# Performance work log

Measured on AMD Instinct MI355X. Metric: run time of the kernel, lower is better.

The kernel has to match this reference:

```python
import jax, jax.numpy as jnp
import numpy as np

B, N, D = 8, 8192, 64          # batch, input points, point feature dim
NPOINT, NSAMPLE = 1024, 16     # FPS samples S, KNN neighbors K
WN, OUT = 16, 128              # weightnet out channels, output channels
CIN = 3 + D                    # concat(xyz_norm, point feats) = linear in_channel
NEG_SLOPE = 0.1


def setup_inputs() -> dict:
    key = jax.random.key(0)
    ks = jax.random.split(key, 8)
    rn = lambda k, shp, s: jax.random.normal(k, shp, jnp.float32) * s
    return {
        "xyz": rn(ks[0], (B, 3, N), 1.0),
        "points": rn(ks[1], (B, D, N), 1.0),
        "w1": rn(ks[2], (3, 8), 0.5), "b1": jnp.zeros((8,), jnp.float32),
        "w2": rn(ks[3], (8, 8), 0.35), "b2": jnp.zeros((8,), jnp.float32),
        "w3": rn(ks[4], (8, WN), 0.35), "b3": jnp.zeros((WN,), jnp.float32),
        "lin_w": rn(ks[5], (WN * CIN, OUT), 0.03),
        "lin_b": jnp.zeros((OUT,), jnp.float32),
    }


def _fps(xyz):
    """Furthest point sampling. xyz: [B,N,3] -> idx [B,NPOINT] int32."""
    def step(carry, _):
        dist, farthest = carry  # [B,N], [B]
        centroid = jnp.take_along_axis(xyz, farthest[:, None, None], axis=1)  # [B,1,3]
        d = jnp.sum((xyz - centroid) ** 2, axis=-1)  # [B,N]
        dist = jnp.minimum(dist, d)
        return (dist, jnp.argmax(dist, axis=-1).astype(jnp.int32)), farthest
    init = (jnp.full((xyz.shape[0], xyz.shape[1]), 1e10, xyz.dtype),
            jnp.zeros((xyz.shape[0],), jnp.int32))
    _, idxs = jax.lax.scan(step, init, None, length=NPOINT)
    return idxs.T  # [B, NPOINT]


def reference(xyz, points, w1, b1, w2, b2, w3, b3, lin_w, lin_b):
    xyz_t = xyz.transpose(0, 2, 1)       # [B,N,3]
    pts_t = points.transpose(0, 2, 1)    # [B,N,D]

    fps_idx = _fps(xyz_t)                                   # [B,S]
    bidx = jnp.arange(B)[:, None]
    new_xyz = xyz_t[bidx, fps_idx]                          # [B,S,3]

    # KNN: squared distances (same ordering as euclidean cdist)
    sqr = jnp.sum((new_xyz[:, :, None, :] - xyz_t[:, None, :, :]) ** 2, axis=-1)  # [B,S,N]
    _, knn = jax.lax.top_k(-sqr, NSAMPLE)                   # [B,S,K]

    b3i = jnp.arange(B)[:, None, None]
    g_xyz = xyz_t[b3i, knn]                                 # [B,S,K,3]
    g_xyz_norm = g_xyz - new_xyz[:, :, None, :]             # [B,S,K,3]
    g_pts = pts_t[b3i, knn]                                 # [B,S,K,D]
    feat = jnp.concatenate([g_xyz_norm, g_pts], axis=-1)    # [B,S,K,3+D]

    # WeightNet: 1x1 convs == per-neighbor MLP on xyz offsets
    h = jax.nn.relu(g_xyz_norm @ w1 + b1)
    h = jax.nn.relu(h @ w2 + b2)
    wts = jax.nn.relu(h @ w3 + b3)                          # [B,S,K,WN]

    # weighted aggregation over K, then flatten [C, WN]
    agg = jnp.einsum('bskc,bskw->bscw', feat, wts).reshape(B, NPOINT, CIN * WN)
    out = agg @ lin_w + lin_b                               # [B,S,OUT]
    out = jnp.where(out > 0, out, NEG_SLOPE * out)          # LeakyReLU(0.1)

    return new_xyz.transpose(0, 2, 1), out.transpose(0, 2, 1), fps_idx
```

## Files before the change

### kernel.cpp

```cpp
#include <hip/hip_runtime.h>
#include <hip/hip_bf16.h>

#define NPTS   8192
#define NBATCH 8
#define S      1024
#define K      16
#define D      64
#define CIN    67
#define WN     16
#define OUTC   128

#define OUT_MAIN 24576
#define OUT_FPS  1073152

#define T_FPS   0
#define T_TP    8
#define T_KNN   1032
#define T_FEAT  1544
#define T_GEMM  2568
#define NBLK    2824

#define SCOPE __HIP_MEMORY_SCOPE_AGENT

typedef float v2f __attribute__((ext_vector_type(2)));

struct Ctrl {
  int ticket;
  int pad0[31];
  int tp_done[8];
  int pad1[24];
  int tile_done[128];
};

__device__ __forceinline__ unsigned long long aload64(const unsigned long long* p) {
  return __hip_atomic_load(p, __ATOMIC_RELAXED, SCOPE);
}
__device__ __forceinline__ void astore64(unsigned long long* p, unsigned long long v) {
  __hip_atomic_store(p, v, __ATOMIC_RELAXED, SCOPE);
}
__device__ __forceinline__ void wait_cnt(int* p, int need) {
  if (threadIdx.x == 0)
    while (__hip_atomic_load(p, __ATOMIC_RELAXED, SCOPE) < need)
      __builtin_amdgcn_s_sleep(4);
  __syncthreads();
}

template <int CTRL, int RM>
__device__ __forceinline__ unsigned long long dpp_max_step(unsigned long long key) {
  int lo = __builtin_amdgcn_update_dpp(0, (int)(unsigned)(key & 0xFFFFFFFFull), CTRL, RM, 0xF, true);
  int hi = __builtin_amdgcn_update_dpp(0, (int)(unsigned)(key >> 32),           CTRL, RM, 0xF, true);
  unsigned long long o = ((unsigned long long)(unsigned)hi << 32) | (unsigned)lo;
  return o > key ? o : key;
}

__device__ void fps_role(int b, const float* __restrict__ xyz,
                         unsigned long long* __restrict__ nxA,
                         unsigned long long* __restrict__ nxB,
                         float* __restrict__ out, void* smem)
{
#pragma clang fp contract(off)
  float* s_x = (float*)smem;
  float* s_y = s_x + NPTS;
  float* s_z = s_y + NPTS;
  float4* hist = (float4*)((char*)smem + 98304);
  unsigned long long* slots = (unsigned long long*)((char*)smem + 114688);

  const int tid  = threadIdx.x;
  const int wave = tid >> 6;
  const int lane = tid & 63;
  const float* xb = xyz + (size_t)b * 3 * NPTS;

  v2f px[8], py[8], pz[8], dist[8];
#pragma unroll
  for (int p = 0; p < 8; p++) {
    int ne = (2 * p) * 512 + tid;
    int no = ne + 512;
    px[p] = (v2f){xb[ne], xb[no]};
    py[p] = (v2f){xb[NPTS + ne], xb[NPTS + no]};
    pz[p] = (v2f){xb[2 * NPTS + ne], xb[2 * NPTS + no]};
    dist[p] = (v2f){1e10f, 1e10f};
    s_x[ne] = px[p].x; s_x[no] = px[p].y;
    s_y[ne] = py[p].x; s_y[no] = py[p].y;
    s_z[ne] = pz[p].x; s_z[no] = pz[p].y;
  }

  int far = 0;
  float cx = xb[0], cy = xb[NPTS], cz = xb[2 * NPTS];

  for (int t = 0; t < 1024; t++) {
    if (tid == (t & 511))
      hist[t] = make_float4(cx, cy, cz, (float)far);

    if ((t & 31) == 0 && t > 0 && wave == 0 && lane < 32) {
      int tt = t - 32 + lane;
      float4 h = hist[tt];
      int gidx = (b << 10) + tt;
      astore64(&nxA[gidx],
               ((unsigned long long)__float_as_uint(h.x) << 32) | __float_as_uint(h.y));
      astore64(&nxB[gidx],
               ((unsigned long long)__float_as_uint(h.z) << 32) | (unsigned)((int)h.w + 1));
    }

    const v2f c2x = (v2f){cx, cx}, c2y = (v2f){cy, cy}, c2z = (v2f){cz, cz};

    float bd_e = -1.0f, bd_o = -1.0f;
    int   ce   = 0,     co   = 0;
#pragma unroll
    for (int p = 0; p < 8; p++) {
      v2f dx = px[p] - c2x, dy = py[p] - c2y, dz = pz[p] - c2z;
      v2f d  = (dx * dx + dy * dy) + dz * dz;
      float nde = fminf(dist[p].x, d.x);
      float ndo = fminf(dist[p].y, d.y);
      dist[p].x = nde;
      dist[p].y = ndo;
      if (nde > bd_e) { bd_e = nde; ce = 2 * p; }
      if (ndo > bd_o) { bd_o = ndo; co = 2 * p + 1; }
    }

    unsigned long long ke =
        ((unsigned long long)__float_as_uint(bd_e) << 32) | (unsigned)(~(unsigned)(ce * 512 + tid));
    unsigned long long ko =
        ((unsigned long long)__float_as_uint(bd_o) << 32) | (unsigned)(~(unsigned)(co * 512 + tid));
    unsigned long long key = ko > ke ? ko : ke;

    key = dpp_max_step<0x111, 0xF>(key);
    key = dpp_max_step<0x112, 0xF>(key);
    key = dpp_max_step<0x114, 0xF>(key);
    key = dpp_max_step<0x118, 0xF>(key);
    key = dpp_max_step<0x142, 0xA>(key);
    key = dpp_max_step<0x143, 0xC>(key);
    if (lane == 63) slots[(t & 1) * 8 + wave] = key;
    __syncthreads();

    const unsigned long long* sl = slots + (t & 1) * 8;
    unsigned long long k0 = sl[0], k1 = sl[1], k2 = sl[2], k3 = sl[3];
    unsigned long long k4 = sl[4], k5 = sl[5], k6 = sl[6], k7 = sl[7];
    k0 = k1 > k0 ? k1 : k0;
    k2 = k3 > k2 ? k3 : k2;
    k4 = k5 > k4 ? k5 : k4;
    k6 = k7 > k6 ? k7 : k6;
    k0 = k2 > k0 ? k2 : k0;
    k4 = k6 > k4 ? k6 : k4;
    k0 = k4 > k0 ? k4 : k0;
    int gi = (int)(~(unsigned)(k0 & 0xFFFFFFFFull));
    far = gi;
    cx = s_x[gi]; cy = s_y[gi]; cz = s_z[gi];
  }
  __syncthreads();

  if (wave == 0 && lane < 32) {
    int tt = 992 + lane;
    float4 h = hist[tt];
    int gidx = (b << 10) + tt;
    astore64(&nxA[gidx],
             ((unsigned long long)__float_as_uint(h.x) << 32) | __float_as_uint(h.y));
    astore64(&nxB[gidx],
             ((unsigned long long)__float_as_uint(h.z) << 32) | (unsigned)((int)h.w + 1));
  }

#pragma unroll
  for (int j = 0; j < 2; j++) {
    int t = j * 512 + tid;
    float4 h = hist[t];
    out[OUT_FPS + b * 1024 + t] = h.w;
    out[b * 3072 + t]           = h.x;
    out[b * 3072 + 1024 + t]    = h.y;
    out[b * 3072 + 2048 + t]    = h.z;
  }
}

__device__ void tp_role(int bid, const float* __restrict__ pts, float* __restrict__ ptt,
                        Ctrl* ctrl, void* smem)
{
  float* tile = (float*)smem;
  const int b  = bid >> 7;
  const int n0 = (bid & 127) * 64;
  const float* pb = pts + (size_t)b * D * NPTS;
#pragma unroll
  for (int i = 0; i < 8; i++) {
    int s = threadIdx.x + i * 512;
    int nl = s & 63, d = s >> 6;
    tile[d * 65 + nl] = pb[(size_t)d * NPTS + n0 + nl];
  }
  __syncthreads();
  float* ob = ptt + ((size_t)b * NPTS + n0) * D;
#pragma unroll
  for (int i = 0; i < 8; i++) {
    int s = threadIdx.x + i * 512;
    int dl = s & 63, nl = s >> 6;
    ob[(size_t)nl * D + dl] = tile[dl * 65 + nl];
  }
  __syncthreads();
  if (threadIdx.x == 0)
    __hip_atomic_fetch_add(&ctrl->tp_done[b], 1, __ATOMIC_RELEASE, SCOPE);
}

__device__ void knn_role(int kidx, const float* __restrict__ xyz,
                         const unsigned long long* __restrict__ nxA,
                         const unsigned long long* __restrict__ nxB,
                         unsigned long long* __restrict__ knnP, void* smem)
{
#pragma clang fp contract(off)
  float (*s_cc)[4] = (float(*)[4])smem;
  unsigned long long* s_k = (unsigned long long*)((char*)smem + 256);
  const int tid   = threadIdx.x;
  const int cl    = tid >> 5;
  const int chunk = tid & 31;
  const int b     = kidx >> 6;
  const int c0    = (kidx & 63) * 16;
  const int cbase = (b << 10) + c0;

  if (chunk == 0) {
    unsigned long long Bv, Av;
    do { Bv = aload64(&nxB[cbase + cl]); } while ((unsigned)(Bv & 0xFFFFFFFFull) == 0u);
    do { Av = aload64(&nxA[cbase + cl]); } while (Av == 0ull);
    s_cc[cl][0] = __uint_as_float((unsigned)(Av >> 32));
    s_cc[cl][1] = __uint_as_float((unsigned)(Av & 0xFFFFFFFFull));
    s_cc[cl][2] = __uint_as_float((unsigned)(Bv >> 32));
  }
  __syncthreads();

  const float* xb = xyz + (size_t)b * 3 * NPTS;
  const float cx = s_cc[cl][0], cy = s_cc[cl][1], cz = s_cc[cl][2];

  float nd[16]; int ni[16];
#pragma unroll
  for (int k = 0; k < 16; k++) { nd[k] = 3.4e38f; ni[k] = 0x7FFFFFFF; }

  for (int jj = 0; jj < 256; jj++) {
    int j = jj * 32 + chunk;
    float dx = xb[j] - cx, dy = xb[NPTS + j] - cy, dz = xb[2 * NPTS + j] - cz;
    float d  = (dx * dx + dy * dy) + dz * dz;
    float cv = d; int iv = j;
#pragma unroll
    for (int k = 0; k < 16; k++) {
      bool sw = cv < nd[k];
      float tv = nd[k]; int ti = ni[k];
      nd[k] = sw ? cv : tv;  ni[k] = sw ? iv : ti;
      cv    = sw ? tv : cv;  iv    = sw ? ti : iv;
    }
  }
#pragma unroll
  for (int k = 0; k < 16; k++)
    s_k[cl * 545 + chunk * 17 + k] =
        ((unsigned long long)__float_as_uint(nd[k]) << 32) | (unsigned)ni[k];
  s_k[cl * 545 + chunk * 17 + 16] = ~0ull;
  __syncthreads();

  if (tid < 16) {
    int pos[32];
#pragma unroll
    for (int c = 0; c < 32; c++) pos[c] = 0;
    int res[16];
    for (int r = 0; r < 16; r++) {
      unsigned long long bk = ~0ull; int bc = 0;
#pragma unroll
      for (int c = 0; c < 32; c++) {
        unsigned long long kv = s_k[tid * 545 + c * 17 + pos[c]];
        if (kv < bk) { bk = kv; bc = c; }
      }
#pragma unroll
      for (int c = 0; c < 32; c++) pos[c] += (c == bc);
      res[r] = (int)(bk & 0xFFFFFFFFull);
    }
#pragma unroll
    for (int w = 0; w < 8; w++)
      astore64(&knnP[(size_t)(cbase + tid) * 8 + w],
               ((unsigned long long)(unsigned)(res[2 * w] + 1) << 32) |
               (unsigned)(res[2 * w + 1] + 1));
  }
}

__device__ void feat_role(int fidx, const float* __restrict__ xyz,
                          const unsigned long long* __restrict__ nxA,
                          const unsigned long long* __restrict__ nxB,
                          const float* __restrict__ ptt,
                          const unsigned long long* __restrict__ knnP,
                          const float* __restrict__ w1, const float* __restrict__ b1,
                          const float* __restrict__ w2, const float* __restrict__ b2,
                          const float* __restrict__ w3, const float* __restrict__ b3,
                          float* __restrict__ agg, Ctrl* ctrl, void* smem)
{
  float* s_wts = (float*)smem;
  float* s_off = s_wts + 8 * 272;
  int*   s_nk  = (int*)(s_off + 8 * 48);

  const int C0 = fidx * 8;
  const int b  = C0 >> 10;

  wait_cnt(&ctrl->tp_done[b], 128);

  const int wv   = threadIdx.x >> 6;
  const int lane = threadIdx.x & 63;
  const int csel = C0 + wv;

  if (lane < 16) {
    const unsigned long long* wp = &knnP[(size_t)csel * 8 + (lane >> 1)];
    unsigned long long wd;
    do { wd = aload64(wp); } while (wd == 0ull);
    unsigned v = (lane & 1) ? (unsigned)(wd & 0xFFFFFFFFull) : (unsigned)(wd >> 32);
    int nk = (int)v - 1;
    s_nk[wv * 16 + lane] = nk;

    unsigned long long Av, Bv;
    do { Av = aload64(&nxA[csel]); } while (Av == 0ull);
    do { Bv = aload64(&nxB[csel]); } while ((unsigned)(Bv & 0xFFFFFFFFull) == 0u);
    float ccx = __uint_as_float((unsigned)(Av >> 32));
    float ccy = __uint_as_float((unsigned)(Av & 0xFFFFFFFFull));
    float ccz = __uint_as_float((unsigned)(Bv >> 32));

    const float* xb = xyz + (size_t)b * 3 * NPTS;
    float ox = xb[nk]            - ccx;
    float oy = xb[NPTS + nk]     - ccy;
    float oz = xb[2 * NPTS + nk] - ccz;
    s_off[wv * 48 + lane * 3 + 0] = ox;
    s_off[wv * 48 + lane * 3 + 1] = oy;
    s_off[wv * 48 + lane * 3 + 2] = oz;
    float h1[8], h2[8];
#pragma unroll
    for (int j = 0; j < 8; j++)
      h1[j] = fmaxf(0.f, ox * w1[j] + oy * w1[8 + j] + oz * w1[16 + j] + b1[j]);
#pragma unroll
    for (int j = 0; j < 8; j++) {
      float a = b2[j];
#pragma unroll
      for (int i = 0; i < 8; i++) a = fmaf(h1[i], w2[i * 8 + j], a);
      h2[j] = fmaxf(0.f, a);
    }
#pragma unroll
    for (int w = 0; w < 16; w++) {
      float a = b3[w];
#pragma unroll
      for (int i = 0; i < 8; i++) a = fmaf(h2[i], w3[i * 16 + w], a);
      s_wts[wv * 272 + lane * 17 + w] = fmaxf(0.f, a);
    }
  }
  __syncthreads();

  float f[16];
#pragma unroll
  for (int k = 0; k < 16; k++) {
    int nk = s_nk[wv * 16 + k];
    f[k] = ptt[((size_t)b * NPTS + nk) * D + lane];
  }

  float acc[16];
#pragma unroll
  for (int w = 0; w < 16; w++) acc[w] = 0.f;
#pragma unroll
  for (int k = 0; k < 16; k++) {
#pragma unroll
    for (int w = 0; w < 16; w++)
      acc[w] = fmaf(f[k], s_wts[wv * 272 + k * 17 + w], acc[w]);
  }
  float* arow = agg + (size_t)csel * (CIN * WN) + (3 + lane) * 16;
#pragma unroll
  for (int q = 0; q < 4; q++) {
    float4 v = make_float4(acc[4 * q], acc[4 * q + 1], acc[4 * q + 2], acc[4 * q + 3]);
    *(float4*)(arow + 4 * q) = v;
  }

  if (lane < 48) {
    int c = lane >> 4, w = lane & 15;
    float a = 0.f;
#pragma unroll
    for (int k = 0; k < 16; k++)
      a = fmaf(s_off[wv * 48 + k * 3 + c], s_wts[wv * 272 + k * 17 + w], a);
    agg[(size_t)csel * (CIN * WN) + c * 16 + w] = a;
  }
  __syncthreads();
  if (threadIdx.x == 0)
    __hip_atomic_fetch_add(&ctrl->tile_done[C0 >> 6], 1, __ATOMIC_RELEASE, SCOPE);
}

__device__ void gemm_role(int gidx, const float* __restrict__ agg, const float* __restrict__ lin_w,
                          const float* __restrict__ lin_b, float* __restrict__ out,
                          Ctrl* ctrl, void* smem)
{
  float* a_t = (float*)smem;
  float* b_t = a_t + 16 * 68;
  const int rt   = gidx >> 1;
  const int ct   = gidx & 1;
  const int row0 = rt * 64;
  const int c0   = ct * 64;

  wait_cnt(&ctrl->tile_done[rt], 8);

  const int tid = threadIdx.x;
  const int cg  = tid & 31;
  const int rg  = tid >> 5;

  float acc[4][2] = {};
  for (int kt = 0; kt < 67; kt++) {
    const int k0 = kt * 16;
#pragma unroll
    for (int i = 0; i < 2; i++) {
      int s = tid + i * 512;
      int kk = s & 15, r = s >> 4;
      a_t[kk * 68 + r] = agg[(size_t)(row0 + r) * (CIN * WN) + k0 + kk];
    }
#pragma unroll
    for (int i = 0; i < 2; i++) {
      int s = tid + i * 512;
      int c = s & 63, kk = s >> 6;
      b_t[kk * 64 + c] = lin_w[(size_t)(k0 + kk) * OUTC + c0 + c];
    }
    __syncthreads();
#pragma unroll
    for (int kk = 0; kk < 16; kk++) {
      const float4 a0 = *(const float4*)&a_t[kk * 68 + rg * 4];
      float bv0 = b_t[kk * 64 + cg * 2];
      float bv1 = b_t[kk * 64 + cg * 2 + 1];
      float av[4] = {a0.x, a0.y, a0.z, a0.w};
#pragma unroll
      for (int rr = 0; rr < 4; rr++) {
        acc[rr][0] = fmaf(av[rr], bv0, acc[rr][0]);
        acc[rr][1] = fmaf(av[rr], bv1, acc[rr][1]);
      }
    }
    __syncthreads();
  }
#pragma unroll
  for (int rr = 0; rr < 4; rr++) {
#pragma unroll
    for (int cc = 0; cc < 2; cc++) {
      int R = row0 + rg * 4 + rr;
      int C = c0 + cg * 2 + cc;
      float v = acc[rr][cc] + lin_b[C];
      v = v > 0.f ? v : 0.1f * v;
      int bb = R >> 10, ss = R & 1023;
      out[OUT_MAIN + ((size_t)(bb * OUTC + C)) * 1024 + ss] = v;
    }
  }
}

__global__ __launch_bounds__(512)
void mega_kernel(const float* __restrict__ xyz, const float* __restrict__ pts,
                 const float* __restrict__ w1, const float* __restrict__ b1,
                 const float* __restrict__ w2, const float* __restrict__ b2,
                 const float* __restrict__ w3, const float* __restrict__ b3,
                 const float* __restrict__ lin_w, const float* __restrict__ lin_b,
                 float* __restrict__ out, unsigned long long* __restrict__ nxA,
                 unsigned long long* __restrict__ nxB, unsigned long long* __restrict__ knnP,
                 float* __restrict__ ptt, float* __restrict__ agg, Ctrl* ctrl)
{
  __shared__ __align__(16) unsigned long long smem[14400];
  __shared__ int s_ticket;
  if (threadIdx.x == 0)
    s_ticket = __hip_atomic_fetch_add(&ctrl->ticket, 1, __ATOMIC_RELAXED, SCOPE);
  __syncthreads();
  const int tk = s_ticket;

  if (tk < T_TP)
    fps_role(tk, xyz, nxA, nxB, out, smem);
  else if (tk < T_KNN)
    tp_role(tk - T_TP, pts, ptt, ctrl, smem);
  else if (tk < T_FEAT)
    knn_role(tk - T_KNN, xyz, nxA, nxB, knnP, smem);
  else if (tk < T_GEMM)
    feat_role(tk - T_FEAT, xyz, nxA, nxB, ptt, knnP,
              w1, b1, w2, b2, w3, b3, agg, ctrl, smem);
  else
    gemm_role(tk - T_GEMM, agg, lin_w, lin_b, out, ctrl, smem);
}

extern "C" void kernel_launch(void* const* d_in, const int* in_sizes, int n_in,
                              void* d_out, int out_size, void* d_ws, size_t ws_size,
                              hipStream_t stream) {
  const float* xyz    = (const float*)d_in[0];
  const float* points = (const float*)d_in[1];
  const float* w1     = (const float*)d_in[2];
  const float* b1     = (const float*)d_in[3];
  const float* w2     = (const float*)d_in[4];
  const float* b2     = (const float*)d_in[5];
  const float* w3     = (const float*)d_in[6];
  const float* b3     = (const float*)d_in[7];
  const float* lin_w  = (const float*)d_in[8];
  const float* lin_b  = (const float*)d_in[9];
  float* out = (float*)d_out;
  char*  ws  = (char*)d_ws;

  Ctrl* ctrl                = (Ctrl*)(ws);
  unsigned long long* nxA   = (unsigned long long*)(ws + 4096);
  unsigned long long* nxB   = (unsigned long long*)(ws + 69632);
  unsigned long long* knnP  = (unsigned long long*)(ws + 135168);
  float* ptt                = (float*)(ws + 1048576);
  float* agg                = (float*)(ws + 17825792);

  hipMemsetAsync(ws, 0, 659456, stream);
  mega_kernel<<<NBLK, 512, 0, stream>>>(xyz, points, w1, b1, w2, b2, w3, b3,
                                        lin_w, lin_b, out, nxA, nxB, knnP, ptt, agg, ctrl);
}
```

Measured before the change: 1.340 ms.

## Fuse KNN, feature aggregation and GEMM into one per-centroid-tile worker role

Replaces the separate KNN, feature and GEMM block roles, which were chained through global flags (knnP, tile_done), with a single worker block per 16-centroid tile. That block does the KNN, keeps the neighbor indices in shared memory, computes the weightnet and aggregation, then runs the final linear layer for its 16 rows. This removes the knnP buffer, the inter-block spin-waits and about half the blocks. In exchange each block reloads the full lin_w for only 16 rows (less reuse than the 64x64 GEMM tiles), and the GEMM tail now sits after each block's KNN on the critical path.

```diff
diff --git a/kernel.cpp b/kernel.cpp
--- a/kernel.cpp
+++ b/kernel.cpp
@@ -15,10 +15,8 @@
 
 #define T_FPS   0
 #define T_TP    8
-#define T_KNN   1032
-#define T_FEAT  1544
-#define T_GEMM  2568
-#define NBLK    2824
+#define T_WK    1032
+#define NBLK    1544
 
 #define SCOPE __HIP_MEMORY_SCOPE_AGENT
 
@@ -28,8 +26,6 @@
   int ticket;
   int pad0[31];
   int tp_done[8];
-  int pad1[24];
-  int tile_done[128];
 };
 
 __device__ __forceinline__ unsigned long long aload64(const unsigned long long* p) {
@@ -37,12 +33,6 @@
 }
 __device__ __forceinline__ void astore64(unsigned long long* p, unsigned long long v) {
   __hip_atomic_store(p, v, __ATOMIC_RELAXED, SCOPE);
-}
-__device__ __forceinline__ void wait_cnt(int* p, int need) {
-  if (threadIdx.x == 0)
-    while (__hip_atomic_load(p, __ATOMIC_RELAXED, SCOPE) < need)
-      __builtin_amdgcn_s_sleep(4);
-  __syncthreads();
 }
 
 template <int CTRL, int RM>
@@ -195,63 +185,77 @@
     __hip_atomic_fetch_add(&ctrl->tp_done[b], 1, __ATOMIC_RELEASE, SCOPE);
 }
 
-__device__ void knn_role(int kidx, const float* __restrict__ xyz,
-                         const unsigned long long* __restrict__ nxA,
-                         const unsigned long long* __restrict__ nxB,
-                         unsigned long long* __restrict__ knnP, void* smem)
+__device__ void worker_role(int u, const float* __restrict__ xyz,
+                            const unsigned long long* __restrict__ nxA,
+                            const unsigned long long* __restrict__ nxB,
+                            const float* __restrict__ ptt,
+                            const float* __restrict__ w1, const float* __restrict__ b1,
+                            const float* __restrict__ w2, const float* __restrict__ b2,
+                            const float* __restrict__ w3, const float* __restrict__ b3,
+                            const float* __restrict__ lin_w, const float* __restrict__ lin_b,
+                            float* __restrict__ agg, float* __restrict__ out,
+                            Ctrl* ctrl, void* smem)
 {
+  const int tid = threadIdx.x;
+  const int b   = u & 7;
+  const int q   = u >> 3;
+  const int c0  = q * 16;
+  const int cbase = (b << 10) + c0;
+
+  unsigned long long* s_k = (unsigned long long*)smem;
+  float* s_cc = (float*)((char*)smem + 69760);
+  int*   s_nk = (int*)((char*)smem + 70016);
+
+  if (tid < 16) {
+    unsigned long long Bv, Av;
+    while ((unsigned)((Bv = aload64(&nxB[cbase + tid])) & 0xFFFFFFFFull) == 0u)
+      __builtin_amdgcn_s_sleep(8);
+    while ((Av = aload64(&nxA[cbase + tid])) == 0ull)
+      __builtin_amdgcn_s_sleep(1);
+    s_cc[tid * 4 + 0] = __uint_as_float((unsigned)(Av >> 32));
+    s_cc[tid * 4 + 1] = __uint_as_float((unsigned)(Av & 0xFFFFFFFFull));
+    s_cc[tid * 4 + 2] = __uint_as_float((unsigned)(Bv >> 32));
+  }
+  __syncthreads();
+
+  {
 #pragma clang fp contract(off)
-  float (*s_cc)[4] = (float(*)[4])smem;
-  unsigned long long* s_k = (unsigned long long*)((char*)smem + 256);
-  const int tid   = threadIdx.x;
-  const int cl    = tid >> 5;
-  const int chunk = tid & 31;
-  const int b     = kidx >> 6;
-  const int c0    = (kidx & 63) * 16;
-  const int cbase = (b << 10) + c0;
-
-  if (chunk == 0) {
-    unsigned long long Bv, Av;
-    do { Bv = aload64(&nxB[cbase + cl]); } while ((unsigned)(Bv & 0xFFFFFFFFull) == 0u);
-    do { Av = aload64(&nxA[cbase + cl]); } while (Av == 0ull);
-    s_cc[cl][0] = __uint_as_float((unsigned)(Av >> 32));
-    s_cc[cl][1] = __uint_as_float((unsigned)(Av & 0xFFFFFFFFull));
-    s_cc[cl][2] = __uint_as_float((unsigned)(Bv >> 32));
-  }
-  __syncthreads();
-
-  const float* xb = xyz + (size_t)b * 3 * NPTS;
-  const float cx = s_cc[cl][0], cy = s_cc[cl][1], cz = s_cc[cl][2];
-
-  float nd[16]; int ni[16];
-#pragma unroll
-  for (int k = 0; k < 16; k++) { nd[k] = 3.4e38f; ni[k] = 0x7FFFFFFF; }
-
-  for (int jj = 0; jj < 256; jj++) {
-    int j = jj * 32 + chunk;
-    float dx = xb[j] - cx, dy = xb[NPTS + j] - cy, dz = xb[2 * NPTS + j] - cz;
-    float d  = (dx * dx + dy * dy) + dz * dz;
-    float cv = d; int iv = j;
-#pragma unroll
-    for (int k = 0; k < 16; k++) {
-      bool sw = cv < nd[k];
-      float tv = nd[k]; int ti = ni[k];
-      nd[k] = sw ? cv : tv;  ni[k] = sw ? iv : ti;
-      cv    = sw ? tv : cv;  iv    = sw ? ti : iv;
-    }
-  }
-#pragma unroll
-  for (int k = 0; k < 16; k++)
-    s_k[cl * 545 + chunk * 17 + k] =
-        ((unsigned long long)__float_as_uint(nd[k]) << 32) | (unsigned)ni[k];
-  s_k[cl * 545 + chunk * 17 + 16] = ~0ull;
+    const int cl    = tid >> 5;
+    const int chunk = tid & 31;
+    const float* xb = xyz + (size_t)b * 3 * NPTS;
+    const float cx = s_cc[cl * 4 + 0];
+    const float cy = s_cc[cl * 4 + 1];
+    const float cz = s_cc[cl * 4 + 2];
+
+    float nd[16]; int ni[16];
+#pragma unroll
+    for (int k = 0; k < 16; k++) { nd[k] = 3.4e38f; ni[k] = 0x7FFFFFFF; }
+
+    for (int jj = 0; jj < 256; jj++) {
+      int j = jj * 32 + chunk;
+      float dx = xb[j] - cx, dy = xb[NPTS + j] - cy, dz = xb[2 * NPTS + j] - cz;
+      float d  = (dx * dx + dy * dy) + dz * dz;
+      float cv = d; int iv = j;
+#pragma unroll
+      for (int k = 0; k < 16; k++) {
+        bool sw = cv < nd[k];
+        float tv = nd[k]; int ti = ni[k];
+        nd[k] = sw ? cv : tv;  ni[k] = sw ? iv : ti;
+        cv    = sw ? tv : cv;  iv    = sw ? ti : iv;
+      }
+    }
+#pragma unroll
+    for (int k = 0; k < 16; k++)
+      s_k[cl * 545 + chunk * 17 + k] =
+          ((unsigned long long)__float_as_uint(nd[k]) << 32) | (unsigned)ni[k];
+    s_k[cl * 545 + chunk * 17 + 16] = ~0ull;
+  }
   __syncthreads();
 
   if (tid < 16) {
     int pos[32];
 #pragma unroll
     for (int c = 0; c < 32; c++) pos[c] = 0;
-    int res[16];
     for (int r = 0; r < 16; r++) {
       unsigned long long bk = ~0ull; int bc = 0;
 #pragma unroll
@@ -261,175 +265,122 @@
       }
 #pragma unroll
       for (int c = 0; c < 32; c++) pos[c] += (c == bc);
-      res[r] = (int)(bk & 0xFFFFFFFFull);
-    }
-#pragma unroll
-    for (int w = 0; w < 8; w++)
-      astore64(&knnP[(size_t)(cbase + tid) * 8 + w],
-               ((unsigned long long)(unsigned)(res[2 * w] + 1) << 32) |
-               (unsigned)(res[2 * w + 1] + 1));
-  }
-}
-
-__device__ void feat_role(int fidx, const float* __restrict__ xyz,
-                          const unsigned long long* __restrict__ nxA,
-                          const unsigned long long* __restrict__ nxB,
-                          const float* __restrict__ ptt,
-                          const unsigned long long* __restrict__ knnP,
-                          const float* __restrict__ w1, const float* __restrict__ b1,
-                          const float* __restrict__ w2, const float* __restrict__ b2,
-                          const float* __restrict__ w3, const float* __restrict__ b3,
-                          float* __restrict__ agg, Ctrl* ctrl, void* smem)
-{
+      s_nk[tid * 16 + r] = (int)(bk & 0xFFFFFFFFull);
+    }
+  }
+  if (tid == 0)
+    while (__hip_atomic_load(&ctrl->tp_done[b], __ATOMIC_RELAXED, SCOPE) < 128)
+      __builtin_amdgcn_s_sleep(8);
+  __syncthreads();
+
   float* s_wts = (float*)smem;
   float* s_off = s_wts + 8 * 272;
-  int*   s_nk  = (int*)(s_off + 8 * 48);
-
-  const int C0 = fidx * 8;
-  const int b  = C0 >> 10;
-
-  wait_cnt(&ctrl->tp_done[b], 128);
-
-  const int wv   = threadIdx.x >> 6;
-  const int lane = threadIdx.x & 63;
-  const int csel = C0 + wv;
-
-  if (lane < 16) {
-    const unsigned long long* wp = &knnP[(size_t)csel * 8 + (lane >> 1)];
-    unsigned long long wd;
-    do { wd = aload64(wp); } while (wd == 0ull);
-    unsigned v = (lane & 1) ? (unsigned)(wd & 0xFFFFFFFFull) : (unsigned)(wd >> 32);
-    int nk = (int)v - 1;
-    s_nk[wv * 16 + lane] = nk;
-
-    unsigned long long Av, Bv;
-    do { Av = aload64(&nxA[csel]); } while (Av == 0ull);
-    do { Bv = aload64(&nxB[csel]); } while ((unsigned)(Bv & 0xFFFFFFFFull) == 0u);
-    float ccx = __uint_as_float((unsigned)(Av >> 32));
-    float ccy = __uint_as_float((unsigned)(Av & 0xFFFFFFFFull));
-    float ccz = __uint_as_float((unsigned)(Bv >> 32));
-
-    const float* xb = xyz + (size_t)b * 3 * NPTS;
-    float ox = xb[nk]            - ccx;
-    float oy = xb[NPTS + nk]     - ccy;
-    float oz = xb[2 * NPTS + nk] - ccz;
-    s_off[wv * 48 + lane * 3 + 0] = ox;
-    s_off[wv * 48 + lane * 3 + 1] = oy;
-    s_off[wv * 48 + lane * 3 + 2] = oz;
-    float h1[8], h2[8];
-#pragma unroll
-    for (int j = 0; j < 8; j++)
-      h1[j] = fmaxf(0.f, ox * w1[j] + oy * w1[8 + j] + oz * w1[16 + j] + b1[j]);
-#pragma unroll
-    for (int j = 0; j < 8; j++) {
-      float a = b2[j];
-#pragma unroll
-      for (int i = 0; i < 8; i++) a = fmaf(h1[i], w2[i * 8 + j], a);
-      h2[j] = fmaxf(0.f, a);
-    }
-#pragma unroll
-    for (int w = 0; w < 16; w++) {
-      float a = b3[w];
-#pragma unroll
-      for (int i = 0; i < 8; i++) a = fmaf(h2[i], w3[i * 16 + w], a);
-      s_wts[wv * 272 + lane * 17 + w] = fmaxf(0.f, a);
-    }
-  }
-  __syncthreads();
-
-  float f[16];
-#pragma unroll
-  for (int k = 0; k < 16; k++) {
-    int nk = s_nk[wv * 16 + k];
-    f[k] = ptt[((size_t)b * NPTS + nk) * D + lane];
-  }
-
-  float acc[16];
-#pragma unroll
-  for (int w = 0; w < 16; w++) acc[w] = 0.f;
-#pragma unroll
-  for (int k = 0; k < 16; k++) {
-#pragma unroll
-    for (int w = 0; w < 16; w++)
-      acc[w] = fmaf(f[k], s_wts[wv * 272 + k * 17 + w], acc[w]);
-  }
-  float* arow = agg + (size_t)csel * (CIN * WN) + (3 + lane) * 16;
-#pragma unroll
-  for (int q = 0; q < 4; q++) {
-    float4 v = make_float4(acc[4 * q], acc[4 * q + 1], acc[4 * q + 2], acc[4 * q + 3]);
-    *(float4*)(arow + 4 * q) = v;
-  }
-
-  if (lane < 48) {
-    int c = lane >> 4, w = lane & 15;
-    float a = 0.f;
-#pragma unroll
-    for (int k = 0; k < 16; k++)
-      a = fmaf(s_off[wv * 48 + k * 3 + c], s_wts[wv * 272 + k * 17 + w], a);
-    agg[(size_t)csel * (CIN * WN) + c * 16 + w] = a;
-  }
-  __syncthreads();
-  if (threadIdx.x == 0)
-    __hip_atomic_fetch_add(&ctrl->tile_done[C0 >> 6], 1, __ATOMIC_RELEASE, SCOPE);
-}
-
-__device__ void gemm_role(int gidx, const float* __restrict__ agg, const float* __restrict__ lin_w,
-                          const float* __restrict__ lin_b, float* __restrict__ out,
-                          Ctrl* ctrl, void* smem)
-{
+  const int wv   = tid >> 6;
+  const int lane = tid & 63;
+
+  for (int it = 0; it < 2; it++) {
+    const int cl2  = it * 8 + wv;
+    const int csel = cbase + cl2;
+    if (lane < 16) {
+      int nk = s_nk[cl2 * 16 + lane];
+      const float* xb = xyz + (size_t)b * 3 * NPTS;
+      float ox = xb[nk]            - s_cc[cl2 * 4 + 0];
+      float oy = xb[NPTS + nk]     - s_cc[cl2 * 4 + 1];
+      float oz = xb[2 * NPTS + nk] - s_cc[cl2 * 4 + 2];
+      s_off[wv * 48 + lane * 3 + 0] = ox;
+      s_off[wv * 48 + lane * 3 + 1] = oy;
+      s_off[wv * 48 + lane * 3 + 2] = oz;
+      float h1[8], h2[8];
+#pragma unroll
+      for (int j = 0; j < 8; j++)
+        h1[j] = fmaxf(0.f, ox * w1[j] + oy * w1[8 + j] + oz * w1[16 + j] + b1[j]);
+#pragma unroll
+      for (int j = 0; j < 8; j++) {
+        float a = b2[j];
+#pragma unroll
+        for (int i = 0; i < 8; i++) a = fmaf(h1[i], w2[i * 8 + j], a);
+        h2[j] = fmaxf(0.f, a);
+      }
+#pragma unroll
+      for (int w = 0; w < 16; w++) {
+        float a = b3[w];
+#pragma unroll
+        for (int i = 0; i < 8; i++) a = fmaf(h2[i], w3[i * 16 + w], a);
+        s_wts[wv * 272 + lane * 17 + w] = fmaxf(0.f, a);
+      }
+    }
+    __syncthreads();
+
+    float f[16];
+#pragma unroll
+    for (int k = 0; k < 16; k++) {
+      int nk = s_nk[cl2 * 16 + k];
+      f[k] = ptt[((size_t)b * NPTS + nk) * D + lane];
+    }
+    float acc[16];
+#pragma unroll
+    for (int w = 0; w < 16; w++) acc[w] = 0.f;
+#pragma unroll
+    for (int k = 0; k < 16; k++) {
+#pragma unroll
+      for (int w = 0; w < 16; w++)
+        acc[w] = fmaf(f[k], s_wts[wv * 272 + k * 17 + w], acc[w]);
+    }
+    float* arow = agg + (size_t)csel * (CIN * WN) + (3 + lane) * 16;
+#pragma unroll
+    for (int qq = 0; qq < 4; qq++) {
+      float4 v = make_float4(acc[4 * qq], acc[4 * qq + 1], acc[4 * qq + 2], acc[4 * qq + 3]);
+      *(float4*)(arow + 4 * qq) = v;
+    }
+    if (lane < 48) {
+      int c = lane >> 4, w = lane & 15;
+      float a = 0.f;
+#pragma unroll
+      for (int k = 0; k < 16; k++)
+        a = fmaf(s_off[wv * 48 + k * 3 + c], s_wts[wv * 272 + k * 17 + w], a);
+      agg[(size_t)csel * (CIN * WN) + c * 16 + w] = a;
+    }
+    __syncthreads();
+  }
+
   float* a_t = (float*)smem;
-  float* b_t = a_t + 16 * 68;
-  const int rt   = gidx >> 1;
-  const int ct   = gidx & 1;
-  const int row0 = rt * 64;
-  const int c0   = ct * 64;
-
-  wait_cnt(&ctrl->tile_done[rt], 8);
-
-  const int tid = threadIdx.x;
-  const int cg  = tid & 31;
-  const int rg  = tid >> 5;
-
-  float acc[4][2] = {};
+  float* b_t = a_t + 16 * 17;
+  float acc2[2][2] = {};
   for (int kt = 0; kt < 67; kt++) {
     const int k0 = kt * 16;
-#pragma unroll
-    for (int i = 0; i < 2; i++) {
-      int s = tid + i * 512;
-      int kk = s & 15, r = s >> 4;
-      a_t[kk * 68 + r] = agg[(size_t)(row0 + r) * (CIN * WN) + k0 + kk];
-    }
-#pragma unroll
-    for (int i = 0; i < 2; i++) {
-      int s = tid + i * 512;
-      int c = s & 63, kk = s >> 6;
-      b_t[kk * 64 + c] = lin_w[(size_t)(k0 + kk) * OUTC + c0 + c];
+    if (tid < 256) {
+      int r = tid & 15, kk = tid >> 4;
+      a_t[kk * 17 + r] = agg[(size_t)(cbase + r) * (CIN * WN) + k0 + kk];
+    }
+#pragma unroll
+    for (int i = 0; i < 4; i++) {
+      int idx = tid + i * 512;
+      int c = idx & 127, kk = idx >> 7;
+      b_t[kk * 128 + c] = lin_w[(size_t)(k0 + kk) * OUTC + c];
     }
     __syncthreads();
 #pragma unroll
     for (int kk = 0; kk < 16; kk++) {
-      const float4 a0 = *(const float4*)&a_t[kk * 68 + rg * 4];
-      float bv0 = b_t[kk * 64 + cg * 2];
-      float bv1 = b_t[kk * 64 + cg * 2 + 1];
-      float av[4] = {a0.x, a0.y, a0.z, a0.w};
-#pragma unroll
-      for (int rr = 0; rr < 4; rr++) {
-        acc[rr][0] = fmaf(av[rr], bv0, acc[rr][0]);
-        acc[rr][1] = fmaf(av[rr], bv1, acc[rr][1]);
-      }
+      float a0 = a_t[kk * 17 + wv * 2];
+      float a1 = a_t[kk * 17 + wv * 2 + 1];
+      float bv0 = b_t[kk * 128 + lane * 2];
+      float bv1 = b_t[kk * 128 + lane * 2 + 1];
+      acc2[0][0] = fmaf(a0, bv0, acc2[0][0]);
+      acc2[0][1] = fmaf(a0, bv1, acc2[0][1]);
+      acc2[1][0] = fmaf(a1, bv0, acc2[1][0]);
+      acc2[1][1] = fmaf(a1, bv1, acc2[1][1]);
     }
     __syncthreads();
   }
 #pragma unroll
-  for (int rr = 0; rr < 4; rr++) {
+  for (int j = 0; j < 2; j++) {
 #pragma unroll
     for (int cc = 0; cc < 2; cc++) {
-      int R = row0 + rg * 4 + rr;
-      int C = c0 + cg * 2 + cc;
-      float v = acc[rr][cc] + lin_b[C];
+      int ss = c0 + wv * 2 + j;
+      int C  = lane * 2 + cc;
+      float v = acc2[j][cc] + lin_b[C];
       v = v > 0.f ? v : 0.1f * v;
-      int bb = R >> 10, ss = R & 1023;
-      out[OUT_MAIN + ((size_t)(bb * OUTC + C)) * 1024 + ss] = v;
+      out[OUT_MAIN + ((size_t)(b * OUTC + C)) * 1024 + ss] = v;
     }
   }
 }
@@ -441,7 +392,7 @@
                  const float* __restrict__ w3, const float* __restrict__ b3,
                  const float* __restrict__ lin_w, const float* __restrict__ lin_b,
                  float* __restrict__ out, unsigned long long* __restrict__ nxA,
-                 unsigned long long* __restrict__ nxB, unsigned long long* __restrict__ knnP,
+                 unsigned long long* __restrict__ nxB,
                  float* __restrict__ ptt, float* __restrict__ agg, Ctrl* ctrl)
 {
   __shared__ __align__(16) unsigned long long smem[14400];
@@ -453,15 +404,11 @@
 
   if (tk < T_TP)
     fps_role(tk, xyz, nxA, nxB, out, smem);
-  else if (tk < T_KNN)
+  else if (tk < T_WK)
     tp_role(tk - T_TP, pts, ptt, ctrl, smem);
-  else if (tk < T_FEAT)
-    knn_role(tk - T_KNN, xyz, nxA, nxB, knnP, smem);
-  else if (tk < T_GEMM)
-    feat_role(tk - T_FEAT, xyz, nxA, nxB, ptt, knnP,
-              w1, b1, w2, b2, w3, b3, agg, ctrl, smem);
   else
-    gemm_role(tk - T_GEMM, agg, lin_w, lin_b, out, ctrl, smem);
+    worker_role(tk - T_WK, xyz, nxA, nxB, ptt, w1, b1, w2, b2, w3, b3,
+                lin_w, lin_b, agg, out, ctrl, smem);
 }
 
 extern "C" void kernel_launch(void* const* d_in, const int* in_sizes, int n_in,
@@ -480,14 +427,13 @@
   float* out = (float*)d_out;
   char*  ws  = (char*)d_ws;
 
-  Ctrl* ctrl                = (Ctrl*)(ws);
-  unsigned long long* nxA   = (unsigned long long*)(ws + 4096);
-  unsigned long long* nxB   = (unsigned long long*)(ws + 69632);
-  unsigned long long* knnP  = (unsigned long long*)(ws + 135168);
-  float* ptt                = (float*)(ws + 1048576);
-  float* agg                = (float*)(ws + 17825792);
-
-  hipMemsetAsync(ws, 0, 659456, stream);
+  Ctrl* ctrl              = (Ctrl*)(ws);
+  unsigned long long* nxA = (unsigned long long*)(ws + 4096);
+  unsigned long long* nxB = (unsigned long long*)(ws + 69632);
+  float* ptt              = (float*)(ws + 1048576);
+  float* agg              = (float*)(ws + 17825792);
+
+  hipMemsetAsync(ws, 0, 135168, stream);
   mega_kernel<<<NBLK, 512, 0, stream>>>(xyz, points, w1, b1, w2, b2, w3, b3,
-                                        lin_w, lin_b, out, nxA, nxB, knnP, ptt, agg, ctrl);
-}
+                                        lin_w, lin_b, out, nxA, nxB, ptt, agg, ctrl);
+}
```

After: 1.296 ms. -3.3%, faster.
